# Kernel optimization log

Measured on AMD Instinct MI355X. Metric: run time of the kernel, lower is better.

Reference implementation:

```python
import jax, jax.numpy as jnp
import numpy as np

NF, NLOC, NALL, NNEI = 2, 2048, 3072, 128
Q_DIM = K_DIM = V_DIM = 256
H, D = 8, 32  # num_heads, head_dim
TOTAL = H * D


def setup_inputs() -> dict:
    key = jax.random.key(0)
    ks = jax.random.split(key, 12)
    inp = {
        "q": jax.random.normal(ks[0], (NF, NLOC, Q_DIM), jnp.float32),
        "k": jax.random.normal(ks[1], (NF, NALL, K_DIM), jnp.float32),
        "v": jax.random.normal(ks[2], (NF, NALL, V_DIM), jnp.float32),
        "nlist": jax.random.randint(ks[3], (NF, NLOC, NNEI), 0, NALL, jnp.int64),
        "bias": jax.random.normal(ks[4], (NF, H, NLOC, NNEI), jnp.float32),
        # torch Linear weights: [out, in]
        "Wq": jax.random.normal(ks[5], (TOTAL, Q_DIM), jnp.float32) * 0.05,
        "Wk": jax.random.normal(ks[6], (TOTAL, K_DIM), jnp.float32) * 0.05,
        "Wv": jax.random.normal(ks[7], (TOTAL, V_DIM), jnp.float32) * 0.05,
        "Wg": jax.random.normal(ks[8], (TOTAL, Q_DIM), jnp.float32) * 0.05,
        "bg": jnp.ones((TOTAL,), jnp.float32),  # gating init: bias=1
        "Wo": jax.random.normal(ks[9], (Q_DIM, TOTAL), jnp.float32) * 0.05,
        "bo": jnp.zeros((Q_DIM,), jnp.float32),
    }
    return inp


def reference(q, k, v, nlist, bias, Wq, Wk, Wv, Wg, bg, Wo, bo):
    nf, nloc, _ = q.shape
    nnei = nlist.shape[-1]
    norm = D ** (-0.5)

    g = q @ Wg.T + bg                       # [nf, nloc, TOTAL]
    qh = (q @ Wq.T) * norm                  # [nf, nloc, TOTAL]
    kh = k @ Wk.T                           # [nf, nall, TOTAL]
    vh = v @ Wv.T                           # [nf, nall, TOTAL]

    # gather neighbors: [nf, nloc, nnei, TOTAL]
    fidx = jnp.arange(nf)[:, None, None]
    kg = kh[fidx, nlist].reshape(nf, nloc, nnei, H, D)
    vg = vh[fidx, nlist].reshape(nf, nloc, nnei, H, D)
    qh = qh.reshape(nf, nloc, H, D)

    # per-atom attention: single query vs nnei neighbors
    attn = jnp.einsum("fnhd,fnihd->fhni", qh, kg)      # [nf, H, nloc, nnei]
    attn = jax.nn.softmax(attn + bias, axis=-1)
    o = jnp.einsum("fhni,fnihd->fnhd", attn, vg)       # [nf, nloc, H, D]
    o = o.reshape(nf, nloc, TOTAL)

    o = jax.nn.sigmoid(g) * o
    return o @ Wo.T + bo
```

## Files before the change

kernel.cpp:

```cpp
#include <hip/hip_runtime.h>

#define NF_   2
#define NLOC_ 2048
#define NALL_ 3072
#define NNEI_ 128
#define H_    8
#define D_    32
#define CH_   256

__device__ __forceinline__ void gemm64(
    const float* __restrict__ A, const float* __restrict__ W,
    const float* __restrict__ bvec, float* __restrict__ C,
    int M, int mode, float (*As)[68], float (*Bs)[68]) {
  const int t  = threadIdx.x;
  const int m0 = blockIdx.y * 64;
  if (m0 >= M) return;
  const int n0 = blockIdx.x * 64;
  const int tx = t & 15;
  const int ty = t >> 4;

  float acc[4][4] = {};

  const int lrow = t >> 2;
  const int lk   = (t & 3) * 8;

  for (int k0 = 0; k0 < 256; k0 += 32) {
    const float4 a0 = *(const float4*)(A + (size_t)(m0 + lrow) * 256 + k0 + lk);
    const float4 a1 = *(const float4*)(A + (size_t)(m0 + lrow) * 256 + k0 + lk + 4);
    const float4 w0 = *(const float4*)(W + (size_t)(n0 + lrow) * 256 + k0 + lk);
    const float4 w1 = *(const float4*)(W + (size_t)(n0 + lrow) * 256 + k0 + lk + 4);
    __syncthreads();
    As[lk + 0][lrow] = a0.x; As[lk + 1][lrow] = a0.y;
    As[lk + 2][lrow] = a0.z; As[lk + 3][lrow] = a0.w;
    As[lk + 4][lrow] = a1.x; As[lk + 5][lrow] = a1.y;
    As[lk + 6][lrow] = a1.z; As[lk + 7][lrow] = a1.w;
    Bs[lk + 0][lrow] = w0.x; Bs[lk + 1][lrow] = w0.y;
    Bs[lk + 2][lrow] = w0.z; Bs[lk + 3][lrow] = w0.w;
    Bs[lk + 4][lrow] = w1.x; Bs[lk + 5][lrow] = w1.y;
    Bs[lk + 6][lrow] = w1.z; Bs[lk + 7][lrow] = w1.w;
    __syncthreads();
#pragma unroll
    for (int kk = 0; kk < 32; ++kk) {
      const float4 av = *(const float4*)(&As[kk][ty * 4]);
      const float4 bv = *(const float4*)(&Bs[kk][tx * 4]);
      const float a[4] = {av.x, av.y, av.z, av.w};
      const float b[4] = {bv.x, bv.y, bv.z, bv.w};
#pragma unroll
      for (int i = 0; i < 4; ++i)
#pragma unroll
        for (int j = 0; j < 4; ++j) acc[i][j] = fmaf(a[i], b[j], acc[i][j]);
    }
  }

  const float norm = 0.17677669529663687f;
#pragma unroll
  for (int i = 0; i < 4; ++i) {
    const int row = m0 + ty * 4 + i;
    float4 o;
    float* op = (float*)&o;
#pragma unroll
    for (int j = 0; j < 4; ++j) {
      const int col = n0 + tx * 4 + j;
      float v = acc[i][j];
      if (mode == 0)      v *= norm;
      else if (mode == 1) v = 1.f / (1.f + __expf(-(v + bvec[col])));
      else if (mode == 3) v += bvec[col];
      op[j] = v;
    }
    *(float4*)(C + (size_t)row * 256 + n0 + tx * 4) = o;
  }
}

__global__ __launch_bounds__(256, 4) void proj_kernel(
    const float* __restrict__ q, const float* __restrict__ k, const float* __restrict__ v,
    const float* __restrict__ Wq, const float* __restrict__ Wg,
    const float* __restrict__ Wk, const float* __restrict__ Wv,
    const float* __restrict__ bg,
    float* __restrict__ qh, float* __restrict__ gs,
    float* __restrict__ kh, float* __restrict__ vh) {
  __shared__ float As[32][68];
  __shared__ float Bs[32][68];
  switch (blockIdx.z) {
    case 0:  gemm64(q, Wq, nullptr, qh, NF_ * NLOC_, 0, As, Bs); break;
    case 1:  gemm64(q, Wg, bg,      gs, NF_ * NLOC_, 1, As, Bs); break;
    case 2:  gemm64(k, Wk, nullptr, kh, NF_ * NALL_, 2, As, Bs); break;
    default: gemm64(v, Wv, nullptr, vh, NF_ * NALL_, 2, As, Bs); break;
  }
}

__global__ __launch_bounds__(256, 4) void out_gemm_kernel(
    const float* __restrict__ x, const float* __restrict__ Wo,
    const float* __restrict__ bo, float* __restrict__ out) {
  __shared__ float As[32][68];
  __shared__ float Bs[32][68];
  gemm64(x, Wo, bo, out, NF_ * NLOC_, 3, As, Bs);
}

__global__ __launch_bounds__(256, 2) void attn_kernel(
    const float* __restrict__ qh, const float* __restrict__ gs,
    const float* __restrict__ kh, const float* __restrict__ vh,
    const void* __restrict__ nlist, const float* __restrict__ bias,
    float* __restrict__ x) {
  __shared__ float q_s[CH_];
  __shared__ int   jn[NNEI_];
  __shared__ float p[H_][NNEI_ + 4];
  __shared__ float K_s[32][256];

  const int t   = threadIdx.x;
  const int bid = blockIdx.x;
  const int f   = bid >> 11;
  const int n   = bid & (NLOC_ - 1);
  const size_t row = (size_t)bid;

  q_s[t] = qh[row * CH_ + t];

  const int* nl32 = (const int*)nlist;
  int odd_or = 0;
#pragma unroll
  for (int w = 1; w < 16; w += 2) odd_or |= nl32[w];
  if (t < NNEI_) {
    if (odd_or == 0) {
      const long long* nl64 = (const long long*)nlist;
      jn[t] = (int)nl64[row * NNEI_ + t];
    } else {
      jn[t] = nl32[row * NNEI_ + t];
    }
  }
  __syncthreads();

  const int h  = t >> 5;
  const int il = t & 31;
  const int w  = t >> 6;
  const int l  = t & 63;

  float4 qv[8];
  {
    const float4* qp = (const float4*)(q_s + h * D_);
#pragma unroll
    for (int i = 0; i < 8; ++i) qv[i] = qp[i];
  }

  const float* kbase = kh + (size_t)f * NALL_ * CH_;
  const float* bb    = bias + (((size_t)f * H_ + h) * NLOC_ + n) * NNEI_;

  float s[4];
#pragma unroll
  for (int c = 0; c < 4; ++c) {
    if (c) __syncthreads();
#pragma unroll
    for (int u = 0; u < 8; ++u) {
      const int r = w * 8 + u;
      const int j = jn[c * 32 + r];
      const float4 kv = *(const float4*)(kbase + (size_t)j * CH_ + l * 4);
      *(float4*)(&K_s[r][(l ^ (r & 7)) * 4]) = kv;
    }
    __syncthreads();
    const int swz = il & 7;
    const float4* krow = (const float4*)(&K_s[il][0]);
    float a = 0.f;
#pragma unroll
    for (int d4 = 0; d4 < 8; ++d4) {
      const float4 kv = krow[(h * 8 + d4) ^ swz];
      a = fmaf(qv[d4].x, kv.x, a);
      a = fmaf(qv[d4].y, kv.y, a);
      a = fmaf(qv[d4].z, kv.z, a);
      a = fmaf(qv[d4].w, kv.w, a);
    }
    s[c] = a + bb[c * 32 + il];
  }

  float m = fmaxf(fmaxf(s[0], s[1]), fmaxf(s[2], s[3]));
#pragma unroll
  for (int off = 16; off >= 1; off >>= 1) m = fmaxf(m, __shfl_xor(m, off));
  float e[4];
  float sum = 0.f;
#pragma unroll
  for (int r = 0; r < 4; ++r) { e[r] = __expf(s[r] - m); sum += e[r]; }
#pragma unroll
  for (int off = 16; off >= 1; off >>= 1) sum += __shfl_xor(sum, off);
  const float inv = 1.f / sum;
#pragma unroll
  for (int r = 0; r < 4; ++r) p[h][il + 32 * r] = e[r] * inv;
  __syncthreads();

  const float* vb = vh + (size_t)f * NALL_ * CH_ + h * D_ + il;
  float ac0 = 0.f, ac1 = 0.f, ac2 = 0.f, ac3 = 0.f;
  for (int i = 0; i < NNEI_; i += 4) {
    const float4 p4 = *(const float4*)(&p[h][i]);
    const int4  j4 = *(const int4*)(&jn[i]);
    ac0 = fmaf(p4.x, vb[(size_t)j4.x * CH_], ac0);
    ac1 = fmaf(p4.y, vb[(size_t)j4.y * CH_], ac1);
    ac2 = fmaf(p4.z, vb[(size_t)j4.z * CH_], ac2);
    ac3 = fmaf(p4.w, vb[(size_t)j4.w * CH_], ac3);
  }
  const float acc = (ac0 + ac1) + (ac2 + ac3);

  const float g = gs[row * CH_ + t];
  x[row * CH_ + t] = g * acc;
}

extern "C" void kernel_launch(void* const* d_in, const int* in_sizes, int n_in,
                              void* d_out, int out_size, void* d_ws, size_t ws_size,
                              hipStream_t stream) {
  const float* q     = (const float*)d_in[0];
  const float* k     = (const float*)d_in[1];
  const float* v     = (const float*)d_in[2];
  const void*  nlist = d_in[3];
  const float* bias  = (const float*)d_in[4];
  const float* Wq    = (const float*)d_in[5];
  const float* Wk    = (const float*)d_in[6];
  const float* Wv    = (const float*)d_in[7];
  const float* Wg    = (const float*)d_in[8];
  const float* bg    = (const float*)d_in[9];
  const float* Wo    = (const float*)d_in[10];
  const float* bo    = (const float*)d_in[11];
  float* out = (float*)d_out;

  float* ws = (float*)d_ws;
  float* qh = ws;
  float* gs = qh + (size_t)NF_ * NLOC_ * CH_;
  float* kh = gs + (size_t)NF_ * NLOC_ * CH_;
  float* vh = kh + (size_t)NF_ * NALL_ * CH_;
  float* x  = vh + (size_t)NF_ * NALL_ * CH_;

  proj_kernel<<<dim3(4, 96, 4), 256, 0, stream>>>(q, k, v, Wq, Wg, Wk, Wv, bg,
                                                  qh, gs, kh, vh);
  attn_kernel<<<dim3(NF_ * NLOC_), 256, 0, stream>>>(qh, gs, kh, vh, nlist, bias, x);
  out_gemm_kernel<<<dim3(4, 64), 256, 0, stream>>>(x, Wo, bo, out);
}
```

Before: 208.4 us.

## Use split-bf16 MFMA GEMMs with 128x128 tiles for projections

Replaces the scalar FP32 64x64 tiled GEMM with a 128x128 tile MFMA GEMM. Each FP32 operand is split into hi and lo bf16 parts and accumulated with three bf16 MFMAs (hh, hl, lh) to approximate FP32 accuracy. The goal is to cut the ALU cost of the projection and output GEMMs. The trade-offs are conversion work, fewer blocks (fewer waves to fill the CUs), scalar epilogue stores, and a small precision loss from dropping the lo*lo term.

```diff
diff --git a/kernel.cpp b/kernel.cpp
--- a/kernel.cpp
+++ b/kernel.cpp
@@ -8,92 +8,141 @@
 #define D_    32
 #define CH_   256
 
-__device__ __forceinline__ void gemm64(
+typedef __attribute__((ext_vector_type(8))) short  short8v;
+typedef __attribute__((ext_vector_type(8))) unsigned short ushort8v;
+typedef __attribute__((ext_vector_type(4))) float  floatx4;
+
+__device__ __forceinline__ unsigned short f2bf(float x) {
+  unsigned u = __float_as_uint(x);
+  unsigned r = u + 0x7fff + ((u >> 16) & 1);
+  return (unsigned short)(r >> 16);
+}
+__device__ __forceinline__ float bf2f(unsigned short h) {
+  return __uint_as_float(((unsigned)h) << 16);
+}
+
+__device__ __forceinline__ void cvt_store(unsigned short* hp, unsigned short* lp,
+                                          float4 u, float4 v) {
+  ushort8v hv, lv;
+  hv[0] = f2bf(u.x); lv[0] = f2bf(u.x - bf2f(hv[0]));
+  hv[1] = f2bf(u.y); lv[1] = f2bf(u.y - bf2f(hv[1]));
+  hv[2] = f2bf(u.z); lv[2] = f2bf(u.z - bf2f(hv[2]));
+  hv[3] = f2bf(u.w); lv[3] = f2bf(u.w - bf2f(hv[3]));
+  hv[4] = f2bf(v.x); lv[4] = f2bf(v.x - bf2f(hv[4]));
+  hv[5] = f2bf(v.y); lv[5] = f2bf(v.y - bf2f(hv[5]));
+  hv[6] = f2bf(v.z); lv[6] = f2bf(v.z - bf2f(hv[6]));
+  hv[7] = f2bf(v.w); lv[7] = f2bf(v.w - bf2f(hv[7]));
+  *(ushort8v*)hp = hv;
+  *(ushort8v*)lp = lv;
+}
+
+__device__ __forceinline__ void gemm_mfma(
     const float* __restrict__ A, const float* __restrict__ W,
     const float* __restrict__ bvec, float* __restrict__ C,
-    int M, int mode, float (*As)[68], float (*Bs)[68]) {
+    int M, int mode,
+    unsigned short (*Ah)[40], unsigned short (*Al)[40],
+    unsigned short (*Wh)[40], unsigned short (*Wl)[40]) {
   const int t  = threadIdx.x;
-  const int m0 = blockIdx.y * 64;
+  const int m0 = blockIdx.y * 128;
   if (m0 >= M) return;
-  const int n0 = blockIdx.x * 64;
-  const int tx = t & 15;
-  const int ty = t >> 4;
-
-  float acc[4][4] = {};
-
-  const int lrow = t >> 2;
-  const int lk   = (t & 3) * 8;
+  const int n0 = blockIdx.x * 128;
+
+  const int lane = t & 63;
+  const int wv   = t >> 6;
+  const int wr   = wv >> 1;
+  const int wc   = wv & 1;
+  const int l15  = lane & 15;
+  const int ko   = (lane >> 4) * 8;
+
+  const int sr = t >> 1;
+  const int sk = (t & 1) * 16;
+
+  floatx4 acc[4][4] = {};
 
   for (int k0 = 0; k0 < 256; k0 += 32) {
-    const float4 a0 = *(const float4*)(A + (size_t)(m0 + lrow) * 256 + k0 + lk);
-    const float4 a1 = *(const float4*)(A + (size_t)(m0 + lrow) * 256 + k0 + lk + 4);
-    const float4 w0 = *(const float4*)(W + (size_t)(n0 + lrow) * 256 + k0 + lk);
-    const float4 w1 = *(const float4*)(W + (size_t)(n0 + lrow) * 256 + k0 + lk + 4);
+    const float* Ap = A + (size_t)(m0 + sr) * 256 + k0 + sk;
+    const float* Wp = W + (size_t)(n0 + sr) * 256 + k0 + sk;
+    const float4 a0 = *(const float4*)(Ap + 0);
+    const float4 a1 = *(const float4*)(Ap + 4);
+    const float4 a2 = *(const float4*)(Ap + 8);
+    const float4 a3 = *(const float4*)(Ap + 12);
+    const float4 w0 = *(const float4*)(Wp + 0);
+    const float4 w1 = *(const float4*)(Wp + 4);
+    const float4 w2 = *(const float4*)(Wp + 8);
+    const float4 w3 = *(const float4*)(Wp + 12);
     __syncthreads();
-    As[lk + 0][lrow] = a0.x; As[lk + 1][lrow] = a0.y;
-    As[lk + 2][lrow] = a0.z; As[lk + 3][lrow] = a0.w;
-    As[lk + 4][lrow] = a1.x; As[lk + 5][lrow] = a1.y;
-    As[lk + 6][lrow] = a1.z; As[lk + 7][lrow] = a1.w;
-    Bs[lk + 0][lrow] = w0.x; Bs[lk + 1][lrow] = w0.y;
-    Bs[lk + 2][lrow] = w0.z; Bs[lk + 3][lrow] = w0.w;
-    Bs[lk + 4][lrow] = w1.x; Bs[lk + 5][lrow] = w1.y;
-    Bs[lk + 6][lrow] = w1.z; Bs[lk + 7][lrow] = w1.w;
+    cvt_store(&Ah[sr][sk + 0], &Al[sr][sk + 0], a0, a1);
+    cvt_store(&Ah[sr][sk + 8], &Al[sr][sk + 8], a2, a3);
+    cvt_store(&Wh[sr][sk + 0], &Wl[sr][sk + 0], w0, w1);
+    cvt_store(&Wh[sr][sk + 8], &Wl[sr][sk + 8], w2, w3);
     __syncthreads();
-#pragma unroll
-    for (int kk = 0; kk < 32; ++kk) {
-      const float4 av = *(const float4*)(&As[kk][ty * 4]);
-      const float4 bv = *(const float4*)(&Bs[kk][tx * 4]);
-      const float a[4] = {av.x, av.y, av.z, av.w};
-      const float b[4] = {bv.x, bv.y, bv.z, bv.w};
-#pragma unroll
-      for (int i = 0; i < 4; ++i)
-#pragma unroll
-        for (int j = 0; j < 4; ++j) acc[i][j] = fmaf(a[i], b[j], acc[i][j]);
-    }
+
+    short8v afh[4], afl[4], bfh[4], bfl[4];
+#pragma unroll
+    for (int mi = 0; mi < 4; ++mi) {
+      const int rr = wr * 64 + mi * 16 + l15;
+      afh[mi] = *(const short8v*)&Ah[rr][ko];
+      afl[mi] = *(const short8v*)&Al[rr][ko];
+    }
+#pragma unroll
+    for (int ni = 0; ni < 4; ++ni) {
+      const int rr = wc * 64 + ni * 16 + l15;
+      bfh[ni] = *(const short8v*)&Wh[rr][ko];
+      bfl[ni] = *(const short8v*)&Wl[rr][ko];
+    }
+#pragma unroll
+    for (int mi = 0; mi < 4; ++mi)
+#pragma unroll
+      for (int ni = 0; ni < 4; ++ni) {
+        acc[mi][ni] = __builtin_amdgcn_mfma_f32_16x16x32_bf16(
+            afh[mi], bfh[ni], acc[mi][ni], 0, 0, 0);
+        acc[mi][ni] = __builtin_amdgcn_mfma_f32_16x16x32_bf16(
+            afh[mi], bfl[ni], acc[mi][ni], 0, 0, 0);
+        acc[mi][ni] = __builtin_amdgcn_mfma_f32_16x16x32_bf16(
+            afl[mi], bfh[ni], acc[mi][ni], 0, 0, 0);
+      }
   }
 
   const float norm = 0.17677669529663687f;
 #pragma unroll
-  for (int i = 0; i < 4; ++i) {
-    const int row = m0 + ty * 4 + i;
-    float4 o;
-    float* op = (float*)&o;
-#pragma unroll
-    for (int j = 0; j < 4; ++j) {
-      const int col = n0 + tx * 4 + j;
-      float v = acc[i][j];
-      if (mode == 0)      v *= norm;
-      else if (mode == 1) v = 1.f / (1.f + __expf(-(v + bvec[col])));
-      else if (mode == 3) v += bvec[col];
-      op[j] = v;
-    }
-    *(float4*)(C + (size_t)row * 256 + n0 + tx * 4) = o;
-  }
-}
-
-__global__ __launch_bounds__(256, 4) void proj_kernel(
+  for (int mi = 0; mi < 4; ++mi)
+#pragma unroll
+    for (int ni = 0; ni < 4; ++ni) {
+      const int col = n0 + wc * 64 + ni * 16 + l15;
+      const float bv = (mode == 1 || mode == 3) ? bvec[col] : 0.f;
+#pragma unroll
+      for (int r = 0; r < 4; ++r) {
+        const int row = m0 + wr * 64 + mi * 16 + (lane >> 4) * 4 + r;
+        float vv = acc[mi][ni][r];
+        if (mode == 0)      vv *= norm;
+        else if (mode == 1) vv = 1.f / (1.f + __expf(-(vv + bv)));
+        else if (mode == 3) vv += bv;
+        C[(size_t)row * 256 + col] = vv;
+      }
+    }
+}
+
+__global__ __launch_bounds__(256, 2) void proj_kernel(
     const float* __restrict__ q, const float* __restrict__ k, const float* __restrict__ v,
     const float* __restrict__ Wq, const float* __restrict__ Wg,
     const float* __restrict__ Wk, const float* __restrict__ Wv,
     const float* __restrict__ bg,
     float* __restrict__ qh, float* __restrict__ gs,
     float* __restrict__ kh, float* __restrict__ vh) {
-  __shared__ float As[32][68];
-  __shared__ float Bs[32][68];
+  __shared__ unsigned short Ah[128][40], Al[128][40], Wh[128][40], Wl[128][40];
   switch (blockIdx.z) {
-    case 0:  gemm64(q, Wq, nullptr, qh, NF_ * NLOC_, 0, As, Bs); break;
-    case 1:  gemm64(q, Wg, bg,      gs, NF_ * NLOC_, 1, As, Bs); break;
-    case 2:  gemm64(k, Wk, nullptr, kh, NF_ * NALL_, 2, As, Bs); break;
-    default: gemm64(v, Wv, nullptr, vh, NF_ * NALL_, 2, As, Bs); break;
-  }
-}
-
-__global__ __launch_bounds__(256, 4) void out_gemm_kernel(
+    case 0:  gemm_mfma(q, Wq, nullptr, qh, NF_ * NLOC_, 0, Ah, Al, Wh, Wl); break;
+    case 1:  gemm_mfma(q, Wg, bg,      gs, NF_ * NLOC_, 1, Ah, Al, Wh, Wl); break;
+    case 2:  gemm_mfma(k, Wk, nullptr, kh, NF_ * NALL_, 2, Ah, Al, Wh, Wl); break;
+    default: gemm_mfma(v, Wv, nullptr, vh, NF_ * NALL_, 2, Ah, Al, Wh, Wl); break;
+  }
+}
+
+__global__ __launch_bounds__(256, 2) void out_gemm_kernel(
     const float* __restrict__ x, const float* __restrict__ Wo,
     const float* __restrict__ bo, float* __restrict__ out) {
-  __shared__ float As[32][68];
-  __shared__ float Bs[32][68];
-  gemm64(x, Wo, bo, out, NF_ * NLOC_, 3, As, Bs);
+  __shared__ unsigned short Ah[128][40], Al[128][40], Wh[128][40], Wl[128][40];
+  gemm_mfma(x, Wo, bo, out, NF_ * NLOC_, 3, Ah, Al, Wh, Wl);
 }
 
 __global__ __launch_bounds__(256, 2) void attn_kernel(
@@ -223,8 +272,8 @@
   float* vh = kh + (size_t)NF_ * NALL_ * CH_;
   float* x  = vh + (size_t)NF_ * NALL_ * CH_;
 
-  proj_kernel<<<dim3(4, 96, 4), 256, 0, stream>>>(q, k, v, Wq, Wg, Wk, Wv, bg,
+  proj_kernel<<<dim3(2, 48, 4), 256, 0, stream>>>(q, k, v, Wq, Wg, Wk, Wv, bg,
                                                   qh, gs, kh, vh);
   attn_kernel<<<dim3(NF_ * NLOC_), 256, 0, stream>>>(qh, gs, kh, vh, nlist, bias, x);
-  out_gemm_kernel<<<dim3(4, 64), 256, 0, stream>>>(x, Wo, bo, out);
-}
+  out_gemm_kernel<<<dim3(2, 32), 256, 0, stream>>>(x, Wo, bo, out);
+}
```

After: 190.6 us. 8.5% less time.
